# Kernel optimization log

Measured on AMD Instinct MI355X. Metric: run time of the kernel, lower is better.

The kernel has to match this reference:

```python
import jax, jax.numpy as jnp
from jax import lax
import numpy as np

K = 3          # kernel_size
PAD = 1        # K // 2
MAX_OFFSET = 0.1
EPS = 1e-8


def setup_inputs() -> dict:
    key = jax.random.key(0)
    k0, k1, k2 = jax.random.split(key, 3)
    B, C, H, W = 4, 64, 256, 256
    Cmid = C // 4
    x = jax.random.normal(k0, (B, C, H, W), jnp.float32)
    # offset_predictor: Conv2d(C+9, C//4, 3, pad=1) -> LeakyReLU(0.2) -> Conv2d(C//4, 2, 3, pad=1) -> Tanh
    w1 = jax.random.normal(k1, (Cmid, C + K * K, 3, 3), jnp.float32) * 0.05
    b1 = jnp.zeros((Cmid,), jnp.float32)
    w2 = jax.random.normal(k2, (2, Cmid, 3, 3), jnp.float32) * 0.05
    b2 = jnp.zeros((2,), jnp.float32)
    return {"x": x, "w1": w1, "b1": b1, "w2": w2, "b2": b2}


def _conv2d(x, w, b):
    # NCHW, OIHW, stride 1, pad 1 (SAME for 3x3)
    out = lax.conv_general_dilated(x, w, (1, 1), ((PAD, PAD), (PAD, PAD)),
                                   dimension_numbers=("NCHW", "OIHW", "NCHW"))
    return out + b[None, :, None, None]


def _local_cosine_similarity(x):
    # F.unfold with zero padding: neighbors[k] at spatial shift (di-1, dj-1), row-major k = di*K + dj
    B, C, H, W = x.shape
    xp = jnp.pad(x, ((0, 0), (0, 0), (PAD, PAD), (PAD, PAD)))
    neighbors = jnp.stack([xp[:, :, di:di + H, dj:dj + W]
                           for di in range(K) for dj in range(K)], axis=2)  # (B,C,9,H,W)
    center = x[:, :, None, :, :]                                            # (B,C,1,H,W)
    numerator = jnp.sum(neighbors * center, axis=1)                         # (B,9,H,W)
    center_norm = jnp.sqrt(jnp.sum(x * x, axis=1)) + EPS                    # (B,H,W)
    neighbor_norm = jnp.sqrt(jnp.sum(neighbors * neighbors, axis=1)) + EPS  # (B,9,H,W)
    return numerator / (center_norm[:, None] * neighbor_norm)               # (B,9,H,W)


def _grid_sample_border(x, grid):
    # bilinear, padding_mode='border', align_corners=True; grid: (B,H,W,2) with (gx,gy) in [-1,1]
    B, C, H, W = x.shape
    ix = (grid[..., 0] + 1.0) * 0.5 * (W - 1)
    iy = (grid[..., 1] + 1.0) * 0.5 * (H - 1)
    ix = jnp.clip(ix, 0.0, W - 1)
    iy = jnp.clip(iy, 0.0, H - 1)
    x0f = jnp.floor(ix); y0f = jnp.floor(iy)
    wx = ix - x0f; wy = iy - y0f
    x0 = x0f.astype(jnp.int32); y0 = y0f.astype(jnp.int32)
    x1 = jnp.minimum(x0 + 1, W - 1); y1 = jnp.minimum(y0 + 1, H - 1)

    def gather(img, yy, xx):  # img (C,H,W), yy/xx (H,W) -> (C,H,W)
        return img[:, yy, xx]

    g = jax.vmap(gather)
    v00 = g(x, y0, x0); v01 = g(x, y0, x1)
    v10 = g(x, y1, x0); v11 = g(x, y1, x1)
    wx = wx[:, None]; wy = wy[:, None]  # broadcast over channel dim
    return ((1 - wy) * ((1 - wx) * v00 + wx * v01)
            + wy * ((1 - wx) * v10 + wx * v11))


def reference(x, w1, b1, w2, b2):
    B, C, H, W = x.shape
    sim = _local_cosine_similarity(x)                       # (B,9,H,W)
    features = jnp.concatenate([x, sim], axis=1)            # (B,C+9,H,W)
    h = _conv2d(features, w1, b1)
    h = jnp.where(h >= 0, h, 0.2 * h)                       # LeakyReLU(0.2)
    offset = jnp.tanh(_conv2d(h, w2, b2)) * MAX_OFFSET      # (B,2,H,W)
    gy, gx = jnp.meshgrid(jnp.linspace(-1.0, 1.0, H),
                          jnp.linspace(-1.0, 1.0, W), indexing="ij")
    base_grid = jnp.stack([gx, gy], axis=-1)[None]          # (1,H,W,2)
    offset_grid = base_grid + jnp.transpose(offset, (0, 2, 3, 1))
    return _grid_sample_border(x, offset_grid)
```

## Files before the change

kernel.cpp:

```cpp
#include <hip/hip_runtime.h>
#include <math.h>

#define B 4
#define C 64
#define H 256
#define W 256
#define CMID 16
#define CIN 73
#define HW (H*W)
#define NW (CIN*9*CMID)
#define XS_STRIDE 260
#define XSR 258

__global__ void transpose_w1_kernel(const float* __restrict__ w1, float* __restrict__ wt) {
    int tid = blockIdx.x * blockDim.x + threadIdx.x;
    if (tid >= NW) return;
    int co = tid & (CMID - 1);
    int rest = tid >> 4;
    int ci = rest / 9;
    int k = rest - ci * 9;
    wt[tid] = w1[(co * CIN + ci) * 9 + k];
}

__device__ __forceinline__ void read_patch9(const float* __restrict__ base, float v[9]) {
#pragma unroll
    for (int r = 0; r < 3; ++r) {
        v[r * 3 + 0] = base[r * XSR + 0];
        v[r * 3 + 1] = base[r * XSR + 1];
        v[r * 3 + 2] = base[r * XSR + 2];
    }
}

__global__ __launch_bounds__(256) void sim_kernel(const float* __restrict__ x,
                                                  float* __restrict__ sim) {
    __shared__ float xs[2][4][3 * XSR];

    int bid = blockIdx.x;
    int sb = (bid & 7) * 128 + (bid >> 3);
    int b = sb >> 8;
    int y = sb & 255;
    int tid = threadIdx.x;

    const float* xb = x + (size_t)b * C * HW;

    bool rv[3];
    long off[3];
#pragma unroll
    for (int j = 0; j < 3; ++j) {
        int grow = y - 1 + j;
        rv[j] = (grow >= 0) && (grow < H);
        off[j] = (long)grow * W + tid;
    }

    if (tid < 48) {
        int e = tid & 1;
        int r = (tid >> 1) % 3;
        int q = (tid >> 1) / 3;
        (&xs[0][0][0])[q * (3 * XSR) + r * XSR + (e ? 257 : 0)] = 0.f;
    }

    float dot[9], nsq[9];
    float csq = 0.f;
#pragma unroll
    for (int i = 0; i < 9; ++i) { dot[i] = nsq[i] = 0.f; }

    float p[12];
#pragma unroll
    for (int k = 0; k < 4; ++k)
#pragma unroll
        for (int j = 0; j < 3; ++j)
            p[k * 3 + j] = rv[j] ? xb[(size_t)k * HW + off[j]] : 0.f;

    int cur = 0;
#pragma unroll 1
    for (int cc = 0; cc < C; cc += 4) {
#pragma unroll
        for (int k = 0; k < 4; ++k)
#pragma unroll
            for (int j = 0; j < 3; ++j)
                xs[cur][k][j * XSR + 1 + tid] = p[k * 3 + j];
        __syncthreads();

        if (cc + 4 < C) {
#pragma unroll
            for (int k = 0; k < 4; ++k)
#pragma unroll
                for (int j = 0; j < 3; ++j)
                    p[k * 3 + j] = rv[j] ? xb[(size_t)(cc + 4 + k) * HW + off[j]] : 0.f;
        }

#pragma unroll
        for (int k = 0; k < 4; ++k) {
            float v[9];
            read_patch9(&xs[cur][k][tid], v);
            float cv = v[4];
            csq = fmaf(cv, cv, csq);
#pragma unroll
            for (int kk = 0; kk < 9; ++kk) {
                if (kk == 4) continue;
                dot[kk] = fmaf(cv, v[kk], dot[kk]);
                nsq[kk] = fmaf(v[kk], v[kk], nsq[kk]);
            }
        }
        cur ^= 1;
    }

    dot[4] = csq;
    nsq[4] = csq;
    float cn = sqrtf(csq) + 1e-8f;
    float* so = sim + (size_t)b * 9 * HW + (size_t)y * W + tid;
#pragma unroll
    for (int kk = 0; kk < 9; ++kk)
        so[(size_t)kk * HW] = dot[kk] / (cn * (sqrtf(nsq[kk]) + 1e-8f));
}

__device__ __forceinline__ void conv1_chan1(const float* __restrict__ base,
                                            const float* __restrict__ wch,
                                            float acc[CMID]) {
    float v[9];
    read_patch9(base, v);
#pragma unroll
    for (int k = 0; k < 9; ++k) {
        const float4* w4 = (const float4*)(wch + k * CMID);
        float a = v[k];
        float4 w0 = w4[0], w1 = w4[1], w2 = w4[2], w3 = w4[3];
        acc[0]  = fmaf(a, w0.x, acc[0]);  acc[1]  = fmaf(a, w0.y, acc[1]);
        acc[2]  = fmaf(a, w0.z, acc[2]);  acc[3]  = fmaf(a, w0.w, acc[3]);
        acc[4]  = fmaf(a, w1.x, acc[4]);  acc[5]  = fmaf(a, w1.y, acc[5]);
        acc[6]  = fmaf(a, w1.z, acc[6]);  acc[7]  = fmaf(a, w1.w, acc[7]);
        acc[8]  = fmaf(a, w2.x, acc[8]);  acc[9]  = fmaf(a, w2.y, acc[9]);
        acc[10] = fmaf(a, w2.z, acc[10]); acc[11] = fmaf(a, w2.w, acc[11]);
        acc[12] = fmaf(a, w3.x, acc[12]); acc[13] = fmaf(a, w3.y, acc[13]);
        acc[14] = fmaf(a, w3.z, acc[14]); acc[15] = fmaf(a, w3.w, acc[15]);
    }
}

__global__ __launch_bounds__(256) void conv1_kernel(const float* __restrict__ x,
                                                    const float* __restrict__ sim,
                                                    const float* __restrict__ wt,
                                                    const float* __restrict__ b1,
                                                    float* __restrict__ h) {
    __shared__ float lw[NW];
    __shared__ float xs[2][3 * XSR];

    int tid = threadIdx.x;
    int bid = blockIdx.x;
    int sb = (bid & 7) * 128 + (bid >> 3);
    int b = sb >> 8;
    int y = sb & 255;

#pragma unroll 1
    for (int j = tid; j < NW / 4; j += 256)
        ((float4*)lw)[j] = ((const float4*)wt)[j];

    const float* gx = x + (size_t)b * C * HW;
    const float* gs = sim + (size_t)b * 9 * HW;

    bool rv[3];
    long off[3];
#pragma unroll
    for (int j = 0; j < 3; ++j) {
        int grow = y - 1 + j;
        rv[j] = (grow >= 0) && (grow < H);
        off[j] = (long)grow * W + tid;
    }

    if (tid < 12) {
        int e = tid & 1;
        int r = (tid >> 1) % 3;
        int ch = (tid >> 1) / 3;
        xs[ch][r * XSR + (e ? 257 : 0)] = 0.f;
    }

    float acc[CMID];
#pragma unroll
    for (int co = 0; co < CMID; ++co) acc[co] = b1[co];

    float p[6];
#pragma unroll
    for (int k = 0; k < 2; ++k)
#pragma unroll
        for (int j = 0; j < 3; ++j)
            p[k * 3 + j] = rv[j] ? gx[(size_t)k * HW + off[j]] : 0.f;

#pragma unroll 1
    for (int cc = 0; cc < 72; cc += 2) {
#pragma unroll
        for (int k = 0; k < 2; ++k)
#pragma unroll
            for (int j = 0; j < 3; ++j)
                xs[k][j * XSR + 1 + tid] = p[k * 3 + j];
        __syncthreads();

#pragma unroll
        for (int k = 0; k < 2; ++k) {
            int ci = cc + 2 + k;
            if (ci < CIN) {
                const float* cb = (ci < C) ? (gx + (size_t)ci * HW)
                                           : (gs + (size_t)(ci - C) * HW);
#pragma unroll
                for (int j = 0; j < 3; ++j)
                    p[k * 3 + j] = rv[j] ? cb[off[j]] : 0.f;
            }
        }

        conv1_chan1(&xs[0][tid], lw + (size_t)cc * 144, acc);
        conv1_chan1(&xs[1][tid], lw + (size_t)(cc + 1) * 144, acc);
        __syncthreads();
    }

#pragma unroll
    for (int j = 0; j < 3; ++j)
        xs[0][j * XSR + 1 + tid] = p[j];
    __syncthreads();
    conv1_chan1(&xs[0][tid], lw + (size_t)72 * 144, acc);

    float* ho = h + (size_t)b * CMID * HW + (size_t)y * W + tid;
#pragma unroll
    for (int co = 0; co < CMID; ++co) {
        float v0 = acc[co];
        v0 = v0 >= 0.f ? v0 : 0.2f * v0;
        ho[(size_t)co * HW] = v0;
    }
}

__device__ __forceinline__ void read_patch_lds(const float* __restrict__ xsbuf,
                                               int rl, int px, float v[3][4]) {
    const float* pb = xsbuf + rl * XS_STRIDE + px;
#pragma unroll
    for (int r = 0; r < 3; ++r) {
        float2 p0 = *(const float2*)(pb + r * XS_STRIDE);
        float2 p1 = *(const float2*)(pb + r * XS_STRIDE + 2);
        v[r][0] = p0.x; v[r][1] = p0.y; v[r][2] = p1.x; v[r][3] = p1.y;
    }
}

__global__ __launch_bounds__(256) void offset_kernel(const float* __restrict__ h,
                                                     const float* __restrict__ w2,
                                                     const float* __restrict__ b2,
                                                     float2* __restrict__ off_buf) {
    __shared__ float lw2[CMID * 9 * 2];
    __shared__ float xs[2][4 * XS_STRIDE];

    int tid = threadIdx.x;
    for (int i = tid; i < CMID * 9 * 2; i += 256) {
        int co = i & 1;
        int rest = i >> 1;
        int ci = rest / 9;
        int kk = rest - ci * 9;
        lw2[i] = w2[(co * CMID + ci) * 9 + kk];
    }

    int bid = blockIdx.x;
    int sb = (bid & 7) * 64 + (bid >> 3);
    int b  = sb >> 7;
    int y0 = (sb & 127) << 1;
    int srow = tid >> 6;
    int sx4  = (tid & 63) << 2;
    int rl = tid >> 7;
    int px = (tid & 127) << 1;
    int y  = y0 + rl;

    int grow = y0 - 1 + srow;
    bool gvalid = (grow >= 0) && (grow < H);
    const float* gh = h + (size_t)b * CMID * HW + (size_t)grow * W + sx4;

    if (tid < 16) {
        int bu = tid >> 3, r = (tid >> 1) & 3, e = (tid & 1) ? 257 : 0;
        xs[bu][r * XS_STRIDE + e] = 0.f;
    }

    float s0x = b2[0], s0y = b2[1], s1x = b2[0], s1y = b2[1];

    float4 r4 = make_float4(0.f, 0.f, 0.f, 0.f);
    if (gvalid) r4 = *(const float4*)gh;

    int cur = 0;
#pragma unroll 1
    for (int ci = 0; ci < CMID; ++ci) {
        float* dst = &xs[cur][srow * XS_STRIDE + 1 + sx4];
        dst[0] = r4.x; dst[1] = r4.y; dst[2] = r4.z; dst[3] = r4.w;
        __syncthreads();
        if (ci + 1 < CMID) {
            r4 = make_float4(0.f, 0.f, 0.f, 0.f);
            if (gvalid) r4 = *(const float4*)(gh + (size_t)(ci + 1) * HW);
        }
        float v[3][4];
        read_patch_lds(xs[cur], rl, px, v);
#pragma unroll
        for (int kr = 0; kr < 3; ++kr)
#pragma unroll
            for (int kc = 0; kc < 3; ++kc) {
                float2 wv = *(const float2*)(lw2 + (ci * 9 + kr * 3 + kc) * 2);
                s0x = fmaf(v[kr][kc],     wv.x, s0x);
                s0y = fmaf(v[kr][kc],     wv.y, s0y);
                s1x = fmaf(v[kr][kc + 1], wv.x, s1x);
                s1y = fmaf(v[kr][kc + 1], wv.y, s1y);
            }
        cur ^= 1;
    }

    float ix0 = (float)px       + 0.1f * tanhf(s0x) * (0.5f * (float)(W - 1));
    float iy0 = (float)y        + 0.1f * tanhf(s0y) * (0.5f * (float)(H - 1));
    float ix1 = (float)(px + 1) + 0.1f * tanhf(s1x) * (0.5f * (float)(W - 1));
    float iy1 = (float)y        + 0.1f * tanhf(s1y) * (0.5f * (float)(H - 1));
    ix0 = fminf(fmaxf(ix0, 0.f), (float)(W - 1));
    iy0 = fminf(fmaxf(iy0, 0.f), (float)(H - 1));
    ix1 = fminf(fmaxf(ix1, 0.f), (float)(W - 1));
    iy1 = fminf(fmaxf(iy1, 0.f), (float)(H - 1));

    float4* op = (float4*)(off_buf + (size_t)b * HW + (size_t)y * W + px);
    *op = make_float4(ix0, iy0, ix1, iy1);
}

#define SROWS 35
__global__ __launch_bounds__(256) void sample_kernel(const float* __restrict__ x,
                                                     const float2* __restrict__ off_buf,
                                                     float* __restrict__ out) {
    __shared__ float xs[SROWS * 256];

    int bid = blockIdx.x;
    int sb = (bid & 7) * 16 + (bid >> 3);
    int b  = sb >> 5;
    int ty = sb & 31;
    int cg = blockIdx.y;
    int tid = threadIdx.x;

    int ybase = ty << 3;
    int lo = ybase - 13;

    int a00[8], a01[8], a10[8], a11[8];
    float wx[8], wy[8];
    const float2* ob2 = off_buf + (size_t)b * HW + (size_t)ybase * W + tid;
#pragma unroll
    for (int r = 0; r < 8; ++r) {
        float2 o = ob2[r * W];
        float xf = floorf(o.x), yf = floorf(o.y);
        wx[r] = o.x - xf; wy[r] = o.y - yf;
        int x0 = (int)xf, yy0 = (int)yf;
        int x1 = min(x0 + 1, W - 1), yy1 = min(yy0 + 1, H - 1);
        int r0 = (yy0 - lo) << 8, r1 = (yy1 - lo) << 8;
        a00[r] = r0 + x0; a01[r] = r0 + x1;
        a10[r] = r1 + x0; a11[r] = r1 + x1;
    }

    const float* xb = x + ((size_t)b * C + cg * 4) * HW;
    float* outb = out + ((size_t)b * C + cg * 4) * HW + (size_t)ybase * W + tid;

#pragma unroll 1
    for (int c = 0; c < 4; ++c) {
        __syncthreads();
        const float* src = xb + (size_t)c * HW;
        for (int j = tid; j < SROWS * 64; j += 256) {
            int row = j >> 6, x4 = (j & 63) << 2;
            int grw = min(max(lo + row, 0), H - 1);
            *(float4*)&xs[(row << 8) + x4] = *(const float4*)(src + (size_t)grw * W + x4);
        }
        __syncthreads();
        float* oc = outb + (size_t)c * HW;
#pragma unroll
        for (int r = 0; r < 8; ++r) {
            float v00 = xs[a00[r]], v01 = xs[a01[r]];
            float v10 = xs[a10[r]], v11 = xs[a11[r]];
            float top = fmaf(wx[r], v01 - v00, v00);
            float bot = fmaf(wx[r], v11 - v10, v10);
            oc[r * W] = fmaf(wy[r], bot - top, top);
        }
    }
}

extern "C" void kernel_launch(void* const* d_in, const int* in_sizes, int n_in,
                              void* d_out, int out_size, void* d_ws, size_t ws_size,
                              hipStream_t stream) {
    const float* x  = (const float*)d_in[0];
    const float* w1 = (const float*)d_in[1];
    const float* b1 = (const float*)d_in[2];
    const float* w2 = (const float*)d_in[3];
    const float* b2 = (const float*)d_in[4];
    float* out = (float*)d_out;

    float* ws  = (float*)d_ws;
    float* wt  = ws;
    float* sim = ws + 16384;
    float* h   = sim + (size_t)B * 9 * HW;
    float2* off_buf = (float2*)(h + (size_t)B * CMID * HW);

    transpose_w1_kernel<<<(NW + 255) / 256, 256, 0, stream>>>(w1, wt);

    sim_kernel<<<B * H, 256, 0, stream>>>(x, sim);
    conv1_kernel<<<B * H, 256, 0, stream>>>(x, sim, wt, b1, h);
    offset_kernel<<<512, 256, 0, stream>>>(h, w2, b2, off_buf);
    sample_kernel<<<dim3(128, 16), 256, 0, stream>>>(x, off_buf, out);
}
```

Measured before the change: 276.4 us.

## Compute two output rows per conv1 block and read weights from global

The conv1 kernel now has each thread compute two adjacent output rows, loading a 4-row input patch so weights and overlapping rows are reused across both outputs. The 42 KB shared-memory weight copy is dropped; weights are read through a per-lane (VGPR-offset) global pointer, so they come from cache instead of LDS. The shared input staging is double-buffered so one barrier per channel pair can be removed. Halving the grid to 512 blocks and doubling accumulators raises register pressure and reduces parallelism. Per-lane weight loads may also cost more bandwidth than LDS broadcasts.

```diff
diff --git a/kernel.cpp b/kernel.cpp
--- a/kernel.cpp
+++ b/kernel.cpp
@@ -114,25 +114,41 @@
         so[(size_t)kk * HW] = dot[kk] / (cn * (sqrtf(nsq[kk]) + 1e-8f));
 }
 
-__device__ __forceinline__ void conv1_chan1(const float* __restrict__ base,
+__device__ __forceinline__ void conv1_ch_p2(const float* __restrict__ base,
                                             const float* __restrict__ wch,
-                                            float acc[CMID]) {
-    float v[9];
-    read_patch9(base, v);
-#pragma unroll
-    for (int k = 0; k < 9; ++k) {
-        const float4* w4 = (const float4*)(wch + k * CMID);
-        float a = v[k];
-        float4 w0 = w4[0], w1 = w4[1], w2 = w4[2], w3 = w4[3];
-        acc[0]  = fmaf(a, w0.x, acc[0]);  acc[1]  = fmaf(a, w0.y, acc[1]);
-        acc[2]  = fmaf(a, w0.z, acc[2]);  acc[3]  = fmaf(a, w0.w, acc[3]);
-        acc[4]  = fmaf(a, w1.x, acc[4]);  acc[5]  = fmaf(a, w1.y, acc[5]);
-        acc[6]  = fmaf(a, w1.z, acc[6]);  acc[7]  = fmaf(a, w1.w, acc[7]);
-        acc[8]  = fmaf(a, w2.x, acc[8]);  acc[9]  = fmaf(a, w2.y, acc[9]);
-        acc[10] = fmaf(a, w2.z, acc[10]); acc[11] = fmaf(a, w2.w, acc[11]);
-        acc[12] = fmaf(a, w3.x, acc[12]); acc[13] = fmaf(a, w3.y, acc[13]);
-        acc[14] = fmaf(a, w3.z, acc[14]); acc[15] = fmaf(a, w3.w, acc[15]);
-    }
+                                            float acc0[CMID], float acc1[CMID]) {
+    float v[4][3];
+#pragma unroll
+    for (int r = 0; r < 4; ++r) {
+        v[r][0] = base[r * XSR + 0];
+        v[r][1] = base[r * XSR + 1];
+        v[r][2] = base[r * XSR + 2];
+    }
+#pragma unroll
+    for (int kr = 0; kr < 3; ++kr)
+#pragma unroll
+        for (int kc = 0; kc < 3; ++kc) {
+            const float4* w4 = (const float4*)(wch + (kr * 3 + kc) * CMID);
+            float4 w0 = w4[0], w1 = w4[1], w2 = w4[2], w3 = w4[3];
+            float a0 = v[kr][kc];
+            float a1 = v[kr + 1][kc];
+            acc0[0]  = fmaf(a0, w0.x, acc0[0]);  acc1[0]  = fmaf(a1, w0.x, acc1[0]);
+            acc0[1]  = fmaf(a0, w0.y, acc0[1]);  acc1[1]  = fmaf(a1, w0.y, acc1[1]);
+            acc0[2]  = fmaf(a0, w0.z, acc0[2]);  acc1[2]  = fmaf(a1, w0.z, acc1[2]);
+            acc0[3]  = fmaf(a0, w0.w, acc0[3]);  acc1[3]  = fmaf(a1, w0.w, acc1[3]);
+            acc0[4]  = fmaf(a0, w1.x, acc0[4]);  acc1[4]  = fmaf(a1, w1.x, acc1[4]);
+            acc0[5]  = fmaf(a0, w1.y, acc0[5]);  acc1[5]  = fmaf(a1, w1.y, acc1[5]);
+            acc0[6]  = fmaf(a0, w1.z, acc0[6]);  acc1[6]  = fmaf(a1, w1.z, acc1[6]);
+            acc0[7]  = fmaf(a0, w1.w, acc0[7]);  acc1[7]  = fmaf(a1, w1.w, acc1[7]);
+            acc0[8]  = fmaf(a0, w2.x, acc0[8]);  acc1[8]  = fmaf(a1, w2.x, acc1[8]);
+            acc0[9]  = fmaf(a0, w2.y, acc0[9]);  acc1[9]  = fmaf(a1, w2.y, acc1[9]);
+            acc0[10] = fmaf(a0, w2.z, acc0[10]); acc1[10] = fmaf(a1, w2.z, acc1[10]);
+            acc0[11] = fmaf(a0, w2.w, acc0[11]); acc1[11] = fmaf(a1, w2.w, acc1[11]);
+            acc0[12] = fmaf(a0, w3.x, acc0[12]); acc1[12] = fmaf(a1, w3.x, acc1[12]);
+            acc0[13] = fmaf(a0, w3.y, acc0[13]); acc1[13] = fmaf(a1, w3.y, acc1[13]);
+            acc0[14] = fmaf(a0, w3.z, acc0[14]); acc1[14] = fmaf(a1, w3.z, acc1[14]);
+            acc0[15] = fmaf(a0, w3.w, acc0[15]); acc1[15] = fmaf(a1, w3.w, acc1[15]);
+        }
 }
 
 __global__ __launch_bounds__(256) void conv1_kernel(const float* __restrict__ x,
@@ -140,56 +156,56 @@
                                                     const float* __restrict__ wt,
                                                     const float* __restrict__ b1,
                                                     float* __restrict__ h) {
-    __shared__ float lw[NW];
-    __shared__ float xs[2][3 * XSR];
+    __shared__ float xs[2][2][4 * XSR];
 
     int tid = threadIdx.x;
     int bid = blockIdx.x;
-    int sb = (bid & 7) * 128 + (bid >> 3);
-    int b = sb >> 8;
-    int y = sb & 255;
-
-#pragma unroll 1
-    for (int j = tid; j < NW / 4; j += 256)
-        ((float4*)lw)[j] = ((const float4*)wt)[j];
+    int sb = (bid & 7) * 64 + (bid >> 3);
+    int b  = sb >> 7;
+    int y0 = (sb & 127) << 1;
+
+    int vz;
+    asm volatile("v_mov_b32 %0, 0" : "=v"(vz));
+    const float* wv = wt + vz;
 
     const float* gx = x + (size_t)b * C * HW;
     const float* gs = sim + (size_t)b * 9 * HW;
 
-    bool rv[3];
-    long off[3];
-#pragma unroll
-    for (int j = 0; j < 3; ++j) {
-        int grow = y - 1 + j;
+    bool rv[4];
+    long off[4];
+#pragma unroll
+    for (int j = 0; j < 4; ++j) {
+        int grow = y0 - 1 + j;
         rv[j] = (grow >= 0) && (grow < H);
         off[j] = (long)grow * W + tid;
     }
 
-    if (tid < 12) {
+    if (tid < 32) {
         int e = tid & 1;
-        int r = (tid >> 1) % 3;
-        int ch = (tid >> 1) / 3;
-        xs[ch][r * XSR + (e ? 257 : 0)] = 0.f;
-    }
-
-    float acc[CMID];
-#pragma unroll
-    for (int co = 0; co < CMID; ++co) acc[co] = b1[co];
-
-    float p[6];
+        int r = (tid >> 1) & 3;
+        int q = tid >> 3;
+        (&xs[0][0][0])[q * (4 * XSR) + r * XSR + (e ? 257 : 0)] = 0.f;
+    }
+
+    float acc0[CMID], acc1[CMID];
+#pragma unroll
+    for (int co = 0; co < CMID; ++co) { acc0[co] = b1[co]; acc1[co] = b1[co]; }
+
+    float p[8];
 #pragma unroll
     for (int k = 0; k < 2; ++k)
 #pragma unroll
-        for (int j = 0; j < 3; ++j)
-            p[k * 3 + j] = rv[j] ? gx[(size_t)k * HW + off[j]] : 0.f;
-
+        for (int j = 0; j < 4; ++j)
+            p[k * 4 + j] = rv[j] ? gx[(size_t)k * HW + off[j]] : 0.f;
+
+    int cur = 0;
 #pragma unroll 1
     for (int cc = 0; cc < 72; cc += 2) {
 #pragma unroll
         for (int k = 0; k < 2; ++k)
 #pragma unroll
-            for (int j = 0; j < 3; ++j)
-                xs[k][j * XSR + 1 + tid] = p[k * 3 + j];
+            for (int j = 0; j < 4; ++j)
+                xs[cur][k][j * XSR + 1 + tid] = p[k * 4 + j];
         __syncthreads();
 
 #pragma unroll
@@ -199,28 +215,30 @@
                 const float* cb = (ci < C) ? (gx + (size_t)ci * HW)
                                            : (gs + (size_t)(ci - C) * HW);
 #pragma unroll
-                for (int j = 0; j < 3; ++j)
-                    p[k * 3 + j] = rv[j] ? cb[off[j]] : 0.f;
+                for (int j = 0; j < 4; ++j)
+                    p[k * 4 + j] = rv[j] ? cb[off[j]] : 0.f;
             }
         }
 
-        conv1_chan1(&xs[0][tid], lw + (size_t)cc * 144, acc);
-        conv1_chan1(&xs[1][tid], lw + (size_t)(cc + 1) * 144, acc);
-        __syncthreads();
-    }
-
-#pragma unroll
-    for (int j = 0; j < 3; ++j)
-        xs[0][j * XSR + 1 + tid] = p[j];
+        conv1_ch_p2(&xs[cur][0][tid], wv + (size_t)cc * 144, acc0, acc1);
+        conv1_ch_p2(&xs[cur][1][tid], wv + (size_t)(cc + 1) * 144, acc0, acc1);
+        cur ^= 1;
+    }
+
+#pragma unroll
+    for (int j = 0; j < 4; ++j)
+        xs[cur][0][j * XSR + 1 + tid] = p[j];
     __syncthreads();
-    conv1_chan1(&xs[0][tid], lw + (size_t)72 * 144, acc);
-
-    float* ho = h + (size_t)b * CMID * HW + (size_t)y * W + tid;
+    conv1_ch_p2(&xs[cur][0][tid], wv + (size_t)72 * 144, acc0, acc1);
+
+    float* ho = h + (size_t)b * CMID * HW + (size_t)y0 * W + tid;
 #pragma unroll
     for (int co = 0; co < CMID; ++co) {
-        float v0 = acc[co];
+        float v0 = acc0[co], v1 = acc1[co];
         v0 = v0 >= 0.f ? v0 : 0.2f * v0;
-        ho[(size_t)co * HW] = v0;
+        v1 = v1 >= 0.f ? v1 : 0.2f * v1;
+        ho[(size_t)co * HW]     = v0;
+        ho[(size_t)co * HW + W] = v1;
     }
 }
 
@@ -388,7 +406,7 @@
     transpose_w1_kernel<<<(NW + 255) / 256, 256, 0, stream>>>(w1, wt);
 
     sim_kernel<<<B * H, 256, 0, stream>>>(x, sim);
-    conv1_kernel<<<B * H, 256, 0, stream>>>(x, sim, wt, b1, h);
+    conv1_kernel<<<512, 256, 0, stream>>>(x, sim, wt, b1, h);
     offset_kernel<<<512, 256, 0, stream>>>(h, w2, b2, off_buf);
     sample_kernel<<<dim3(128, 16), 256, 0, stream>>>(x, off_buf, out);
 }
```

Result: slower. 329.7 us (+19.3%).
